# Kernel tuning notes

Hardware: AMD Instinct MI355X
Metric: run time of the kernel (lower is better)

## Reference

```python
import jax, jax.numpy as jnp
import numpy as np

N, D, H, C, E = 16384, 768, 768, 2, 20

def setup_inputs() -> dict:
    key = jax.random.key(0)
    k1, k2, k3, k4, k5, k6 = jax.random.split(key, 6)
    return {
        "embeddings": jax.random.normal(k1, (N, D), dtype=jnp.float32),
        "component_idx": jax.random.randint(k2, (N,), 0, E, dtype=jnp.int64),
        "W1": jax.random.normal(k3, (E, D, H), dtype=jnp.float32) * (1.0 / np.sqrt(D)),
        "b1": jnp.zeros((E, H), dtype=jnp.float32),
        "W2": jax.random.normal(k4, (E, H, C), dtype=jnp.float32) * (1.0 / np.sqrt(H)),
        "b2": jnp.zeros((E, C), dtype=jnp.float32),
    }

def reference(embeddings, component_idx, W1, b1, W2, b2):
    # Each token n goes through expert component_idx[n]:
    #   y = relu(x @ W1[e] + b1[e]) @ W2[e] + b2[e]
    # The torch module's mask/cat/argsort reassembly is mathematically a
    # per-token select of its own expert's output at the original position.
    # Dense-expert formulation (standard jax MoE fallback), then gather.
    h = jax.nn.relu(jnp.einsum('nd,edh->enh', embeddings, W1) + b1[:, None, :])  # [E,N,H]
    y = jnp.einsum('enh,ehc->enc', h, W2) + b2[:, None, :]                        # [E,N,C]
    n_idx = jnp.arange(embeddings.shape[0])
    return y[component_idx, n_idx]  # [N,C]
```

## Files before the change

kernel.cpp:

```cpp
#include <hip/hip_runtime.h>

#define N_D 768
#define N_H 768
#define N_C 2
#define N_E 20
#define MT 128
#define NT 128
#define BK 32
#define KT (N_D / BK)
#define MAX_TILES 160
#define ROWB (N_D * 2)

typedef __attribute__((ext_vector_type(8))) short short8;
typedef __attribute__((ext_vector_type(4))) float f32x4;

__device__ __forceinline__ unsigned short f2bf(float f) {
  unsigned u = __builtin_bit_cast(unsigned, f);
  u += 0x7FFFu + ((u >> 16) & 1u);
  return (unsigned short)(u >> 16);
}

#define GLD_LDS16(gp, lp)                                                        \
  __builtin_amdgcn_global_load_lds(                                              \
      (const __attribute__((address_space(1))) void*)(gp),                       \
      (__attribute__((address_space(3))) void*)(lp), 16, 0, 0)


__global__ __launch_bounds__(256) void k_hist(const int* __restrict__ cidx,
                                              int* __restrict__ counts, int n) {
  __shared__ int lc[N_E];
  if (threadIdx.x < N_E) lc[threadIdx.x] = 0;
  __syncthreads();
  for (int i = blockIdx.x * blockDim.x + threadIdx.x; i < n;
       i += gridDim.x * blockDim.x) {
    int e = cidx[i];
    e = e < 0 ? 0 : (e >= N_E ? N_E - 1 : e);
    atomicAdd(&lc[e], 1);
  }
  __syncthreads();
  if (threadIdx.x < N_E) atomicAdd(&counts[threadIdx.x], lc[threadIdx.x]);
}

__global__ __launch_bounds__(64) void k_scan(const int* __restrict__ counts,
                                             int* __restrict__ offsets,
                                             int* __restrict__ cursor,
                                             int* __restrict__ tiles,
                                             int* __restrict__ numTiles) {
  int t = threadIdx.x;
  if (t < N_E) {
    int run = 0, trun = 0;
    for (int e = 0; e < t; ++e) {
      run += counts[e];
      trun += (counts[e] + MT - 1) / MT;
    }
    offsets[t] = run;
    cursor[t] = run;
    int nt = (counts[t] + MT - 1) / MT;
    for (int m = 0; m < nt; ++m) tiles[trun + m] = (t << 8) | m;
    if (t == N_E - 1) *numTiles = trun + nt;
  }
}

__global__ __launch_bounds__(256) void k_scatter(const int* __restrict__ cidx,
                                                 int* __restrict__ cursor,
                                                 int* __restrict__ sorted, int n) {
  __shared__ int lc[N_E];
  __shared__ int lbase[N_E];
  int tid = threadIdx.x;
  if (tid < N_E) lc[tid] = 0;
  __syncthreads();
  int i = blockIdx.x * blockDim.x + tid;
  int e = 0, p = 0;
  if (i < n) {
    e = cidx[i];
    e = e < 0 ? 0 : (e >= N_E ? N_E - 1 : e);
    p = atomicAdd(&lc[e], 1);
  }
  __syncthreads();
  if (tid < N_E) lbase[tid] = atomicAdd(&cursor[tid], lc[tid]);
  __syncthreads();
  if (i < n) sorted[lbase[e] + p] = i;
}


__global__ __launch_bounds__(192) void k_gather(const float* __restrict__ emb,
                                                const int* __restrict__ sorted,
                                                unsigned short* __restrict__ Xg,
                                                int n) {
  int row = blockIdx.x;
  int j = threadIdx.x;
  ushort4 o;
  if (row < n) {
    float4 v = ((const float4*)(emb + (size_t)sorted[row] * N_D))[j];
    o.x = f2bf(v.x);
    o.y = f2bf(v.y);
    o.z = f2bf(v.z);
    o.w = f2bf(v.w);
  } else {
    o.x = o.y = o.z = o.w = 0;
  }
  ((ushort4*)(Xg + (size_t)row * N_D))[j] = o;
}


__global__ __launch_bounds__(256) void k_w1_cvt(const float* __restrict__ W1,
                                                unsigned short* __restrict__ W1t) {
  __shared__ float tile[64][65];
  int e = blockIdx.z, h0 = blockIdx.x * 64, d0 = blockIdx.y * 64;
  const float* src = W1 + (size_t)e * N_D * N_H;
  unsigned short* dst = W1t + (size_t)e * N_H * N_D;
  int tx = threadIdx.x & 15, ty = threadIdx.x >> 4;
  for (int s = 0; s < 4; ++s) {
    int d = s * 16 + ty;
    float4 v = *(const float4*)&src[(size_t)(d0 + d) * N_H + h0 + tx * 4];
    tile[d][tx * 4 + 0] = v.x;
    tile[d][tx * 4 + 1] = v.y;
    tile[d][tx * 4 + 2] = v.z;
    tile[d][tx * 4 + 3] = v.w;
  }
  __syncthreads();
  int px = threadIdx.x & 7, py = threadIdx.x >> 3;
  for (int s = 0; s < 2; ++s) {
    int h = s * 32 + py;
    short8 v;
    for (int j = 0; j < 8; ++j)
      v[j] = (short)f2bf(tile[px * 8 + j][h]);
    *(short8*)&dst[(size_t)(h0 + h) * N_D + d0 + px * 8] = v;
  }
}


__global__ __launch_bounds__(256, 3) void k_gemm(
    const unsigned short* __restrict__ Xg, const unsigned short* __restrict__ W1t,
    const float* __restrict__ b1, const float* __restrict__ W2,
    const float* __restrict__ b2, const int* __restrict__ sorted,
    const int* __restrict__ counts, const int* __restrict__ offsets,
    const int* __restrict__ tiles, const int* __restrict__ numTiles,
    float* __restrict__ out) {
  const int p = blockIdx.x;
  const int xcd = p & 7;
  const int t = p >> 3;
  const int bx = t % 6;
  const int mth = t / 6;
  const int mt = xcd + 8 * mth;
  if (mt >= *numTiles) return;
  const int tv = tiles[mt];
  const int e = tv >> 8;
  const int m0 = (tv & 255) * MT;
  const int off = offsets[e];
  const int cnt_rel = counts[e] - m0;
  const int n0 = bx * NT;

  __shared__ unsigned short lA[3][MT * BK];
  __shared__ unsigned short lB[3][NT * BK];

  const int tid = threadIdx.x;
  const int wid = tid >> 6, lane = tid & 63;
  const int wm = (wid >> 1) * 64, wn = (wid & 1) * 64;
  const int quad = lane >> 4, lm = lane & 15;

  const int R0 = wid * 32 + lm;
  const char* agp = (const char*)Xg + (size_t)(off + m0 + R0) * ROWB + quad * 16;
  const char* bgp = (const char*)W1t + (size_t)e * N_H * ROWB +
                    (size_t)(n0 + R0) * ROWB + quad * 16;
  unsigned short* lap[3] = {&lA[0][(wid * 32) * BK], &lA[1][(wid * 32) * BK],
                            &lA[2][(wid * 32) * BK]};
  unsigned short* lbp[3] = {&lB[0][(wid * 32) * BK], &lB[1][(wid * 32) * BK],
                            &lB[2][(wid * 32) * BK]};

#define ISSUE_BATCH(kk, b)                                                       \
  do {                                                                           \
    const char* a_ = agp + (kk)*64;                                              \
    const char* b_ = bgp + (kk)*64;                                              \
    GLD_LDS16(a_, lap[b]);                                                       \
    GLD_LDS16(a_ + 16 * ROWB, lap[b] + 16 * BK);                                 \
    GLD_LDS16(b_, lbp[b]);                                                       \
    GLD_LDS16(b_ + 16 * ROWB, lbp[b] + 16 * BK);                                 \
  } while (0)

  f32x4 acc[4][4] = {};

  ISSUE_BATCH(0, 0);
  ISSUE_BATCH(1, 1);
  ISSUE_BATCH(2, 2);

  const int fa = quad * 128 + lm * 8;

#define GEMM_BODY(kt, cur, DO_ISSUE)                                             \
  do {                                                                           \
    short8 af[4], bfr[4];                                                        \
    for (int i = 0; i < 4; ++i)                                                  \
      af[i] = *(const short8*)&lA[cur][((wm >> 4) + i) * 512 + fa];              \
    for (int j = 0; j < 4; ++j)                                                  \
      bfr[j] = *(const short8*)&lB[cur][((wn >> 4) + j) * 512 + fa];             \
    asm volatile("s_waitcnt lgkmcnt(0)\n\ts_barrier" ::: "memory");              \
    if (DO_ISSUE) ISSUE_BATCH((kt) + 3, cur);                                    \
    for (int i = 0; i < 4; ++i)                                                  \
      for (int j = 0; j < 4; ++j)                                                \
        acc[i][j] = __builtin_amdgcn_mfma_f32_16x16x32_bf16(af[i], bfr[j],       \
                                                            acc[i][j], 0, 0, 0); \
  } while (0)

#pragma unroll
  for (int kt = 0; kt < KT - 2; ++kt) {
    const int cur = kt % 3;
    asm volatile("s_waitcnt vmcnt(8)\n\ts_barrier" ::: "memory");
    GEMM_BODY(kt, cur, kt < KT - 3);
  }
  {
    asm volatile("s_waitcnt vmcnt(4)\n\ts_barrier" ::: "memory");
    GEMM_BODY(KT - 2, (KT - 2) % 3, false);
  }
  {
    asm volatile("s_waitcnt vmcnt(0)\n\ts_barrier" ::: "memory");
    GEMM_BODY(KT - 1, (KT - 1) % 3, false);
  }

  float y0[4][4], y1[4][4];
  for (int i = 0; i < 4; ++i)
    for (int r = 0; r < 4; ++r) y0[i][r] = y1[i][r] = 0.f;

  for (int j = 0; j < 4; ++j) {
    int col = n0 + wn + j * 16 + lm;
    float bias = b1[e * N_H + col];
    float2 w2 = *(const float2*)&W2[((size_t)e * N_H + col) * N_C];
    for (int i = 0; i < 4; ++i) {
      f32x4 a = acc[i][j];
      for (int r = 0; r < 4; ++r) {
        float h = a[r] + bias;
        h = h > 0.f ? h : 0.f;
        y0[i][r] += h * w2.x;
        y1[i][r] += h * w2.y;
      }
    }
  }
  for (int s = 1; s < 16; s <<= 1) {
    for (int i = 0; i < 4; ++i)
      for (int r = 0; r < 4; ++r) {
        y0[i][r] += __shfl_xor(y0[i][r], s, 64);
        y1[i][r] += __shfl_xor(y1[i][r], s, 64);
      }
  }
  if (lm == 0) {
    const bool add_bias = (n0 == 0) && (wn == 0);
    float bb0 = add_bias ? b2[e * N_C + 0] : 0.f;
    float bb1 = add_bias ? b2[e * N_C + 1] : 0.f;
    for (int i = 0; i < 4; ++i) {
      for (int r = 0; r < 4; ++r) {
        int mrel = wm + i * 16 + quad * 4 + r;
        if (mrel < cnt_rel) {
          int token = sorted[off + m0 + mrel];
          atomicAdd(&out[(size_t)token * N_C + 0], y0[i][r] + bb0);
          atomicAdd(&out[(size_t)token * N_C + 1], y1[i][r] + bb1);
        }
      }
    }
  }
}


extern "C" void kernel_launch(void* const* d_in, const int* in_sizes, int n_in,
                              void* d_out, int out_size, void* d_ws, size_t ws_size,
                              hipStream_t stream) {
  const float* emb = (const float*)d_in[0];
  const int* cidx = (const int*)d_in[1];
  const float* W1 = (const float*)d_in[2];
  const float* b1 = (const float*)d_in[3];
  const float* W2 = (const float*)d_in[4];
  const float* b2 = (const float*)d_in[5];
  float* out = (float*)d_out;
  const int n = in_sizes[1];

  char* ws = (char*)d_ws;
  int* counts = (int*)ws;
  int* offsets = (int*)(ws + 128);
  int* cursor = (int*)(ws + 256);
  int* numTiles = (int*)(ws + 384);
  int* tiles = (int*)(ws + 512);
  int* sorted = (int*)(ws + 2048);
  size_t sorted_bytes = ((size_t)n * 4 + 255) & ~(size_t)255;
  unsigned short* Xg = (unsigned short*)(ws + 2048 + sorted_bytes);
  int pcap = n + MT;
  unsigned short* W1t = Xg + (size_t)pcap * N_D;

  hipMemsetAsync(d_ws, 0, 2048, stream);
  hipMemsetAsync(d_out, 0, (size_t)out_size * sizeof(float), stream);
  int nb = (n + 255) / 256;
  k_hist<<<nb, 256, 0, stream>>>(cidx, counts, n);
  k_scan<<<1, 64, 0, stream>>>(counts, offsets, cursor, tiles, numTiles);
  k_scatter<<<nb, 256, 0, stream>>>(cidx, cursor, sorted, n);
  k_gather<<<pcap, 192, 0, stream>>>(emb, sorted, Xg, n);
  k_w1_cvt<<<dim3(N_H / 64, N_D / 64, N_E), 256, 0, stream>>>(W1, W1t);
  k_gemm<<<8 * 6 * (MAX_TILES / 8), 256, 0, stream>>>(
      Xg, W1t, b1, W2, b2, sorted, counts, offsets, tiles, numTiles, out);
}
```

Measured before the change: 231.0 us.

## Map expert tiles to XCDs by expert and shrink LDS pipeline to double buffer

The scan kernel now builds a per-XCD slot table that assigns each expert (e mod 8) to one XCD, listing all of its M-tiles and N-blocks. Every block on an XCD then reads the same expert's W1 slice, which should improve L2 reuse of the weights. The GEMM also drops from a triple-buffered to a double-buffered LDS pipeline and raises launch bounds to 4 blocks per CU. This trades prefetch depth for occupancy, and the fixed 160-slot cap per XCD could silently drop tiles if one XCD's experts exceed it.

Result: faster. 224.6 us (-2.7%).

```diff
diff --git a/kernel.cpp b/kernel.cpp
--- a/kernel.cpp
+++ b/kernel.cpp
@@ -8,8 +8,8 @@
 #define NT 128
 #define BK 32
 #define KT (N_D / BK)
-#define MAX_TILES 160
 #define ROWB (N_D * 2)
+#define SLOTMAX 160
 
 typedef __attribute__((ext_vector_type(8))) short short8;
 typedef __attribute__((ext_vector_type(4))) float f32x4;
@@ -44,20 +44,23 @@
 __global__ __launch_bounds__(64) void k_scan(const int* __restrict__ counts,
                                              int* __restrict__ offsets,
                                              int* __restrict__ cursor,
-                                             int* __restrict__ tiles,
-                                             int* __restrict__ numTiles) {
+                                             int* __restrict__ slots) {
   int t = threadIdx.x;
   if (t < N_E) {
-    int run = 0, trun = 0;
-    for (int e = 0; e < t; ++e) {
-      run += counts[e];
-      trun += (counts[e] + MT - 1) / MT;
-    }
+    int run = 0;
+    for (int e = 0; e < t; ++e) run += counts[e];
     offsets[t] = run;
     cursor[t] = run;
-    int nt = (counts[t] + MT - 1) / MT;
-    for (int m = 0; m < nt; ++m) tiles[trun + m] = (t << 8) | m;
-    if (t == N_E - 1) *numTiles = trun + nt;
+  }
+  if (t < 8) {
+    int idx = 0;
+    for (int e = t; e < N_E; e += 8) {
+      int nt = (counts[e] + MT - 1) / MT;
+      for (int m = 0; m < nt; ++m)
+        for (int bx = 0; bx < 6; ++bx)
+          if (idx < SLOTMAX) slots[t * SLOTMAX + idx++] = e | (m << 8) | (bx << 16);
+    }
+    for (; idx < SLOTMAX; ++idx) slots[t * SLOTMAX + idx] = -1;
   }
 }
 
@@ -130,29 +133,23 @@
 }
 
 
-__global__ __launch_bounds__(256, 3) void k_gemm(
+__global__ __launch_bounds__(256, 4) void k_gemm(
     const unsigned short* __restrict__ Xg, const unsigned short* __restrict__ W1t,
     const float* __restrict__ b1, const float* __restrict__ W2,
     const float* __restrict__ b2, const int* __restrict__ sorted,
     const int* __restrict__ counts, const int* __restrict__ offsets,
-    const int* __restrict__ tiles, const int* __restrict__ numTiles,
-    float* __restrict__ out) {
+    const int* __restrict__ slots, float* __restrict__ out) {
   const int p = blockIdx.x;
-  const int xcd = p & 7;
-  const int t = p >> 3;
-  const int bx = t % 6;
-  const int mth = t / 6;
-  const int mt = xcd + 8 * mth;
-  if (mt >= *numTiles) return;
-  const int tv = tiles[mt];
-  const int e = tv >> 8;
-  const int m0 = (tv & 255) * MT;
+  const int sv = slots[(p & 7) * SLOTMAX + (p >> 3)];
+  if (sv < 0) return;
+  const int e = sv & 255;
+  const int m0 = ((sv >> 8) & 255) * MT;
+  const int n0 = (sv >> 16) * NT;
   const int off = offsets[e];
   const int cnt_rel = counts[e] - m0;
-  const int n0 = bx * NT;
-
-  __shared__ unsigned short lA[3][MT * BK];
-  __shared__ unsigned short lB[3][NT * BK];
+
+  __shared__ unsigned short lA[2][MT * BK];
+  __shared__ unsigned short lB[2][NT * BK];
 
   const int tid = threadIdx.x;
   const int wid = tid >> 6, lane = tid & 63;
@@ -163,10 +160,8 @@
   const char* agp = (const char*)Xg + (size_t)(off + m0 + R0) * ROWB + quad * 16;
   const char* bgp = (const char*)W1t + (size_t)e * N_H * ROWB +
                     (size_t)(n0 + R0) * ROWB + quad * 16;
-  unsigned short* lap[3] = {&lA[0][(wid * 32) * BK], &lA[1][(wid * 32) * BK],
-                            &lA[2][(wid * 32) * BK]};
-  unsigned short* lbp[3] = {&lB[0][(wid * 32) * BK], &lB[1][(wid * 32) * BK],
-                            &lB[2][(wid * 32) * BK]};
+  unsigned short* lap[2] = {&lA[0][(wid * 32) * BK], &lA[1][(wid * 32) * BK]};
+  unsigned short* lbp[2] = {&lB[0][(wid * 32) * BK], &lB[1][(wid * 32) * BK]};
 
 #define ISSUE_BATCH(kk, b)                                                       \
   do {                                                                           \
@@ -182,7 +177,6 @@
 
   ISSUE_BATCH(0, 0);
   ISSUE_BATCH(1, 1);
-  ISSUE_BATCH(2, 2);
 
   const int fa = quad * 128 + lm * 8;
 
@@ -194,7 +188,7 @@
     for (int j = 0; j < 4; ++j)                                                  \
       bfr[j] = *(const short8*)&lB[cur][((wn >> 4) + j) * 512 + fa];             \
     asm volatile("s_waitcnt lgkmcnt(0)\n\ts_barrier" ::: "memory");              \
-    if (DO_ISSUE) ISSUE_BATCH((kt) + 3, cur);                                    \
+    if (DO_ISSUE) ISSUE_BATCH((kt) + 2, cur);                                    \
     for (int i = 0; i < 4; ++i)                                                  \
       for (int j = 0; j < 4; ++j)                                                \
         acc[i][j] = __builtin_amdgcn_mfma_f32_16x16x32_bf16(af[i], bfr[j],       \
@@ -202,18 +196,14 @@
   } while (0)
 
 #pragma unroll
-  for (int kt = 0; kt < KT - 2; ++kt) {
-    const int cur = kt % 3;
-    asm volatile("s_waitcnt vmcnt(8)\n\ts_barrier" ::: "memory");
-    GEMM_BODY(kt, cur, kt < KT - 3);
-  }
-  {
+  for (int kt = 0; kt < KT - 1; ++kt) {
+    const int cur = kt & 1;
     asm volatile("s_waitcnt vmcnt(4)\n\ts_barrier" ::: "memory");
-    GEMM_BODY(KT - 2, (KT - 2) % 3, false);
+    GEMM_BODY(kt, cur, kt < KT - 2);
   }
   {
     asm volatile("s_waitcnt vmcnt(0)\n\ts_barrier" ::: "memory");
-    GEMM_BODY(KT - 1, (KT - 1) % 3, false);
+    GEMM_BODY(KT - 1, (KT - 1) & 1, false);
   }
 
   float y0[4][4], y1[4][4];
@@ -275,22 +265,21 @@
   int* counts = (int*)ws;
   int* offsets = (int*)(ws + 128);
   int* cursor = (int*)(ws + 256);
-  int* numTiles = (int*)(ws + 384);
-  int* tiles = (int*)(ws + 512);
-  int* sorted = (int*)(ws + 2048);
+  int* slots = (int*)(ws + 1024);
+  int* sorted = (int*)(ws + 8192);
   size_t sorted_bytes = ((size_t)n * 4 + 255) & ~(size_t)255;
-  unsigned short* Xg = (unsigned short*)(ws + 2048 + sorted_bytes);
+  unsigned short* Xg = (unsigned short*)(ws + 8192 + sorted_bytes);
   int pcap = n + MT;
   unsigned short* W1t = Xg + (size_t)pcap * N_D;
 
-  hipMemsetAsync(d_ws, 0, 2048, stream);
+  hipMemsetAsync(d_ws, 0, 1024, stream);
   hipMemsetAsync(d_out, 0, (size_t)out_size * sizeof(float), stream);
   int nb = (n + 255) / 256;
   k_hist<<<nb, 256, 0, stream>>>(cidx, counts, n);
-  k_scan<<<1, 64, 0, stream>>>(counts, offsets, cursor, tiles, numTiles);
+  k_scan<<<1, 64, 0, stream>>>(counts, offsets, cursor, slots);
   k_scatter<<<nb, 256, 0, stream>>>(cidx, cursor, sorted, n);
   k_gather<<<pcap, 192, 0, stream>>>(emb, sorted, Xg, n);
   k_w1_cvt<<<dim3(N_H / 64, N_D / 64, N_E), 256, 0, stream>>>(W1, W1t);
-  k_gemm<<<8 * 6 * (MAX_TILES / 8), 256, 0, stream>>>(
-      Xg, W1t, b1, W2, b2, sorted, counts, offsets, tiles, numTiles, out);
-}
+  k_gemm<<<8 * SLOTMAX, 256, 0, stream>>>(Xg, W1t, b1, W2, b2, sorted, counts,
+                                          offsets, slots, out);
+}
```
